# Kernel optimization log

Measured on AMD Instinct MI355X. Metric: run time of the kernel, lower is better.

The kernel has to match this reference:

```python
import jax, jax.numpy as jnp
import numpy as np

D_MODEL = 1024
NUM_HEADS = 16
D_K = D_MODEL // NUM_HEADS
SCALE = float(np.sqrt(D_K))


def setup_inputs() -> dict:
    key = jax.random.key(0)
    ks = jax.random.split(key, 12)
    B, S = 4, 2048
    s = 1.0 / np.sqrt(D_MODEL)
    inp = {
        'query': jax.random.normal(ks[0], (B, S, D_MODEL), jnp.float32),
        'key':   jax.random.normal(ks[1], (B, S, D_MODEL), jnp.float32),
        'value': jax.random.normal(ks[2], (B, S, D_MODEL), jnp.float32),
        'Wq': jax.random.normal(ks[3], (D_MODEL, D_MODEL), jnp.float32) * s,
        'bq': jax.random.normal(ks[4], (D_MODEL,), jnp.float32) * s,
        'Wk': jax.random.normal(ks[5], (D_MODEL, D_MODEL), jnp.float32) * s,
        'bk': jax.random.normal(ks[6], (D_MODEL,), jnp.float32) * s,
        'Wv': jax.random.normal(ks[7], (D_MODEL, D_MODEL), jnp.float32) * s,
        'bv': jax.random.normal(ks[8], (D_MODEL,), jnp.float32) * s,
        'Wo': jax.random.normal(ks[9], (D_MODEL, D_MODEL), jnp.float32) * s,
        'bo': jax.random.normal(ks[10], (D_MODEL,), jnp.float32) * s,
    }
    return inp


def reference(query, key, value, Wq, bq, Wk, bk, Wv, bv, Wo, bo):
    B, Sq, _ = query.shape
    Skv = key.shape[1]
    # torch Linear: x @ W.T + b
    def proj(x, W, b, S):
        y = jnp.einsum('bsd,ed->bse', x, W) + b
        return y.reshape(B, S, NUM_HEADS, D_K).transpose(0, 2, 1, 3)  # [B,H,S,dk]
    Q = proj(query, Wq, bq, Sq)
    K = proj(key, Wk, bk, Skv)
    V = proj(value, Wv, bv, Skv)
    scores = jnp.einsum('bhqd,bhkd->bhqk', Q, K) / SCALE  # [B,H,Sq,Skv]
    attn = jax.nn.softmax(scores, axis=-1)  # dropout=0 -> identity
    out = jnp.einsum('bhqk,bhkd->bhqd', attn, V)
    out = out.transpose(0, 2, 1, 3).reshape(B, Sq, D_MODEL)
    out = jnp.einsum('bsd,ed->bse', out, Wo) + bo
    return out
```

## Files before the change

kernel.cpp:

```cpp
#include <hip/hip_runtime.h>


typedef __attribute__((ext_vector_type(8))) __bf16 bf16x8;
typedef __attribute__((ext_vector_type(4))) __bf16 bf16x4;
typedef __attribute__((ext_vector_type(4))) float f32x4;

#define SCALE_FOLD 0.18033688011112043f

__device__ __forceinline__ void async_copy16(const void* g, void* lds) {
  __builtin_amdgcn_global_load_lds(
      (const __attribute__((address_space(1))) void*)g,
      (__attribute__((address_space(3))) void*)lds, 16, 0, 0);
}

template <int ROWS>
__device__ __forceinline__ void stage_tile(const __bf16* __restrict__ g, int ld,
                                           __bf16* lds, int tid) {
  const int wave_base = tid & ~63;
#pragma unroll
  for (int r = 0; r < ROWS / 32; ++r) {
    int slot = r * 256 + tid;
    int row = slot >> 3;
    int c = slot & 7;
    int gc = c ^ (row & 7);
    async_copy16(g + row * ld + gc * 8, lds + (r * 256 + wave_base) * 8);
  }
}

__device__ __forceinline__ bf16x8 frag_ld(const __bf16* lds, int row, int chunk) {
  return *(const bf16x8*)(lds + row * 64 + ((chunk ^ (row & 7)) << 3));
}

__global__ void cvt3(const float* __restrict__ s0, const float* __restrict__ s1,
                     const float* __restrict__ s2, __bf16* d0, __bf16* d1,
                     __bf16* d2, int n4) {
  const float* src = blockIdx.y == 0 ? s0 : (blockIdx.y == 1 ? s1 : s2);
  __bf16* dst = blockIdx.y == 0 ? d0 : (blockIdx.y == 1 ? d1 : d2);
  int i = blockIdx.x * blockDim.x + threadIdx.x;
  if (i < n4) {
    float4 v = ((const float4*)src)[i];
    bf16x4 o = {(__bf16)v.x, (__bf16)v.y, (__bf16)v.z, (__bf16)v.w};
    ((bf16x4*)dst)[i] = o;
  }
}

__global__ void cvt4(const float* __restrict__ s0, const float* __restrict__ s1,
                     const float* __restrict__ s2, const float* __restrict__ s3,
                     __bf16* d0, __bf16* d1, __bf16* d2, __bf16* d3, int n4) {
  const float* src = blockIdx.y == 0 ? s0
                     : (blockIdx.y == 1 ? s1 : (blockIdx.y == 2 ? s2 : s3));
  __bf16* dst =
      blockIdx.y == 0 ? d0 : (blockIdx.y == 1 ? d1 : (blockIdx.y == 2 ? d2 : d3));
  int i = blockIdx.x * blockDim.x + threadIdx.x;
  if (i < n4) {
    float4 v = ((const float4*)src)[i];
    bf16x4 o = {(__bf16)v.x, (__bf16)v.y, (__bf16)v.z, (__bf16)v.w};
    ((bf16x4*)dst)[i] = o;
  }
}

__device__ __forceinline__ void gemm_body(const __bf16* __restrict__ A,
                                          const __bf16* __restrict__ B,
                                          const float* __restrict__ bias,
                                          void* __restrict__ out, int K,
                                          int mode, int m0, int n0,
                                          __bf16* Alds, __bf16* Blds) {
  const int tid = threadIdx.x;
  const int lane = tid & 63;
  const int w = tid >> 6;
  const int wm = w >> 1, wn = w & 1;
  const int l15 = lane & 15, quad = lane >> 4;

  f32x4 acc[4][4] = {};

  for (int k0 = 0; k0 < K; k0 += 64) {
    stage_tile<128>(A + m0 * K + k0, K, Alds, tid);
    stage_tile<128>(B + n0 * K + k0, K, Blds, tid);
    __syncthreads();
#pragma unroll
    for (int kc = 0; kc < 2; ++kc) {
      bf16x8 af[4], bfr[4];
#pragma unroll
      for (int mi = 0; mi < 4; ++mi)
        af[mi] = frag_ld(Alds, wm * 64 + mi * 16 + l15, kc * 4 + quad);
#pragma unroll
      for (int ni = 0; ni < 4; ++ni)
        bfr[ni] = frag_ld(Blds, wn * 64 + ni * 16 + l15, kc * 4 + quad);
#pragma unroll
      for (int mi = 0; mi < 4; ++mi)
#pragma unroll
        for (int ni = 0; ni < 4; ++ni)
          acc[mi][ni] = __builtin_amdgcn_mfma_f32_16x16x32_bf16(
              af[mi], bfr[ni], acc[mi][ni], 0, 0, 0);
    }
    __syncthreads();
  }

#pragma unroll
  for (int mi = 0; mi < 4; ++mi) {
#pragma unroll
    for (int i = 0; i < 4; ++i) {
      int grow = m0 + wm * 64 + mi * 16 + quad * 4 + i;
#pragma unroll
      for (int ni = 0; ni < 4; ++ni) {
        int gcol = n0 + wn * 64 + ni * 16 + l15;
        float v = acc[mi][ni][i];
        if (mode == 3) {
          v += bias[gcol];
          ((float*)out)[grow * 1024 + gcol] = v;
        } else if (mode == 2) {
          v += bias[grow];
          int h = grow >> 6, dd = grow & 63;
          int b = gcol >> 11, s = gcol & 2047;
          ((__bf16*)out)[(((b * 16 + h) * 64 + dd) * 2048) + s] = (__bf16)v;
        } else {
          v += bias[gcol];
          if (mode == 0) v *= SCALE_FOLD;
          int h = gcol >> 6, dd = gcol & 63;
          int b = grow >> 11, s = grow & 2047;
          ((__bf16*)out)[(((b * 16 + h) * 2048 + s) * 64) + dd] = (__bf16)v;
        }
      }
    }
  }
}

__global__ __launch_bounds__(256) void gemm_qkv(
    const __bf16* __restrict__ xq, const __bf16* __restrict__ xk,
    const __bf16* __restrict__ xv, const __bf16* __restrict__ wq,
    const __bf16* __restrict__ wk, const __bf16* __restrict__ wv,
    const float* __restrict__ bq, const float* __restrict__ bk,
    const float* __restrict__ bv, __bf16* Qb, __bf16* Kb, __bf16* Vtb) {
  __shared__ alignas(16) __bf16 Alds[128 * 64];
  __shared__ alignas(16) __bf16 Blds[128 * 64];
  const int z = blockIdx.z;
  if (z == 0) {
    gemm_body(xq, wq, bq, Qb, 1024, 0, blockIdx.y * 128, blockIdx.x * 128,
              Alds, Blds);
  } else if (z == 1) {
    gemm_body(xk, wk, bk, Kb, 1024, 1, blockIdx.y * 128, blockIdx.x * 128,
              Alds, Blds);
  } else {
    gemm_body(wv, xv, bv, Vtb, 1024, 2, blockIdx.x * 128, blockIdx.y * 128,
              Alds, Blds);
  }
}

__global__ __launch_bounds__(256) void gemm_out(const __bf16* __restrict__ A,
                                                const __bf16* __restrict__ B,
                                                const float* __restrict__ bias,
                                                float* __restrict__ out) {
  __shared__ alignas(16) __bf16 Alds[128 * 64];
  __shared__ alignas(16) __bf16 Blds[128 * 64];
  gemm_body(A, B, bias, out, 1024, 3, blockIdx.y * 128, blockIdx.x * 128, Alds,
            Blds);
}

__global__ __launch_bounds__(256, 2) void attn_kernel(
    const __bf16* __restrict__ Qg, const __bf16* __restrict__ Kg,
    const __bf16* __restrict__ Vt, __bf16* __restrict__ AO) {
  __shared__ alignas(16) __bf16 Klds[2][64 * 64];
  __shared__ alignas(16) __bf16 Vlds[2][64 * 64];
  __shared__ alignas(16) __bf16 PQ[256 * 64];

  const int tid = threadIdx.x;
  const int lane = tid & 63;
  const int w = tid >> 6;
  const int l15 = lane & 15, quad = lane >> 4;
  const int bh = blockIdx.y;
  const int q0 = blockIdx.x * 256;
  const int S = 2048;

  const __bf16* Qbase = Qg + (size_t)bh * S * 64;
  const __bf16* Kbase = Kg + (size_t)bh * S * 64;
  const __bf16* Vbase = Vt + (size_t)bh * 64 * S;

  stage_tile<256>(Qbase + q0 * 64, 64, PQ, tid);
  stage_tile<64>(Kbase, 64, Klds[0], tid);
  stage_tile<64>(Vbase, S, Vlds[0], tid);
  __syncthreads();
  bf16x8 qf[4][2];
#pragma unroll
  for (int qi = 0; qi < 4; ++qi)
#pragma unroll
    for (int kc = 0; kc < 2; ++kc)
      qf[qi][kc] = frag_ld(PQ, w * 64 + qi * 16 + l15, kc * 4 + quad);
  __syncthreads();

  const bf16x8 ones = {__bf16(1.f), __bf16(1.f), __bf16(1.f), __bf16(1.f),
                       __bf16(1.f), __bf16(1.f), __bf16(1.f), __bf16(1.f)};

  f32x4 oacc[4][4] = {};
  f32x4 lacc[4] = {};

  __bf16* Pw = PQ + w * 64 * 64;

  for (int t = 0; t < 32; ++t) {
    const int cur = t & 1;
    if (t + 1 < 32) {
      stage_tile<64>(Kbase + (t + 1) * 64 * 64, 64, Klds[cur ^ 1], tid);
      stage_tile<64>(Vbase + (t + 1) * 64, S, Vlds[cur ^ 1], tid);
    }

    f32x4 sacc[4][4] = {};
#pragma unroll
    for (int kc = 0; kc < 2; ++kc) {
      bf16x8 kf[4];
#pragma unroll
      for (int ci = 0; ci < 4; ++ci)
        kf[ci] = frag_ld(Klds[cur], ci * 16 + l15, kc * 4 + quad);
#pragma unroll
      for (int ci = 0; ci < 4; ++ci)
#pragma unroll
        for (int qi = 0; qi < 4; ++qi)
          sacc[ci][qi] = __builtin_amdgcn_mfma_f32_16x16x32_bf16(
              kf[ci], qf[qi][kc], sacc[ci][qi], 0, 0, 0);
    }

#pragma unroll
    for (int ci = 0; ci < 4; ++ci) {
#pragma unroll
      for (int qi = 0; qi < 4; ++qi) {
        bf16x4 pk;
#pragma unroll
        for (int i = 0; i < 4; ++i)
          pk[i] = (__bf16)__builtin_amdgcn_exp2f(sacc[ci][qi][i]);
        int qrow = qi * 16 + l15;
        int addr = qrow * 64 + (((2 * ci + (quad >> 1)) ^ (qrow & 7)) << 3) +
                   ((quad & 1) << 2);
        *(bf16x4*)(Pw + addr) = pk;
      }
    }

#pragma unroll
    for (int kc = 0; kc < 2; ++kc) {
      bf16x8 pf[4], vf[4];
#pragma unroll
      for (int mi = 0; mi < 4; ++mi)
        pf[mi] = frag_ld(Pw, mi * 16 + l15, kc * 4 + quad);
#pragma unroll
      for (int ni = 0; ni < 4; ++ni)
        vf[ni] = frag_ld(Vlds[cur], ni * 16 + l15, kc * 4 + quad);
#pragma unroll
      for (int mi = 0; mi < 4; ++mi)
        lacc[mi] = __builtin_amdgcn_mfma_f32_16x16x32_bf16(pf[mi], ones,
                                                           lacc[mi], 0, 0, 0);
#pragma unroll
      for (int mi = 0; mi < 4; ++mi)
#pragma unroll
        for (int ni = 0; ni < 4; ++ni)
          oacc[mi][ni] = __builtin_amdgcn_mfma_f32_16x16x32_bf16(
              pf[mi], vf[ni], oacc[mi][ni], 0, 0, 0);
    }
    __syncthreads();
  }

  const int b = bh >> 4;
  const int hh = bh & 15;
#pragma unroll
  for (int mi = 0; mi < 4; ++mi) {
#pragma unroll
    for (int i = 0; i < 4; ++i) {
      int s = q0 + w * 64 + mi * 16 + quad * 4 + i;
      float inv_l = 1.f / lacc[mi][i];
#pragma unroll
      for (int ni = 0; ni < 4; ++ni) {
        int d = ni * 16 + l15;
        AO[((size_t)(b * 2048 + s)) * 1024 + hh * 64 + d] =
            (__bf16)(oacc[mi][ni][i] * inv_l);
      }
    }
  }
}

extern "C" void kernel_launch(void* const* d_in, const int* in_sizes, int n_in,
                              void* d_out, int out_size, void* d_ws,
                              size_t ws_size, hipStream_t stream) {
  const float* q_in = (const float*)d_in[0];
  const float* k_in = (const float*)d_in[1];
  const float* v_in = (const float*)d_in[2];
  const float* Wq = (const float*)d_in[3];
  const float* bq = (const float*)d_in[4];
  const float* Wk = (const float*)d_in[5];
  const float* bk = (const float*)d_in[6];
  const float* Wv = (const float*)d_in[7];
  const float* bv = (const float*)d_in[8];
  const float* Wo = (const float*)d_in[9];
  const float* bo = (const float*)d_in[10];

  const size_t SZ_X = (size_t)8192 * 1024 * 2;
  const size_t SZ_W = (size_t)1024 * 1024 * 2;
  char* p = (char*)d_ws;
  __bf16* xq = (__bf16*)p; p += SZ_X;
  __bf16* xk = (__bf16*)p; p += SZ_X;
  __bf16* xv = (__bf16*)p; p += SZ_X;
  __bf16* wqb = (__bf16*)p; p += SZ_W;
  __bf16* wkb = (__bf16*)p; p += SZ_W;
  __bf16* wvb = (__bf16*)p; p += SZ_W;
  __bf16* wob = (__bf16*)p; p += SZ_W;
  __bf16* Qb = (__bf16*)p; p += SZ_X;
  __bf16* Kb = (__bf16*)p; p += SZ_X;
  __bf16* Vtb = (__bf16*)p; p += SZ_X;
  __bf16* AOb = (__bf16*)p; p += SZ_X;

  const int nx4 = 8192 * 1024 / 4, nw4 = 1024 * 1024 / 4;
  cvt3<<<dim3(nx4 / 256, 3), 256, 0, stream>>>(q_in, k_in, v_in, xq, xk, xv,
                                               nx4);
  cvt4<<<dim3(nw4 / 256, 4), 256, 0, stream>>>(Wq, Wk, Wv, Wo, wqb, wkb, wvb,
                                               wob, nw4);

  gemm_qkv<<<dim3(8, 64, 3), 256, 0, stream>>>(xq, xk, xv, wqb, wkb, wvb, bq,
                                               bk, bv, Qb, Kb, Vtb);

  attn_kernel<<<dim3(8, 64), 256, 0, stream>>>(Qb, Kb, Vtb, AOb);

  gemm_out<<<dim3(8, 64), 256, 0, stream>>>(AOb, wob, bo, (float*)d_out);
}
```

Before: 345.8 us.

## Halve attention query tile per block, split KV tile into sub-steps, merge convert kernels

The attention kernel now handles 128 queries per block (32 per wave) instead of 256. It processes each 64-key tile as two 32-key sub-steps with a much smaller per-wave P buffer in LDS, which cuts LDS use and accumulator registers and doubles the grid to 1024 blocks. This aims for more resident blocks and better CU balance, at the cost of reloading K/V tiles for twice as many blocks and using smaller MFMA batches per step. The two fp32-to-bf16 convert kernels are merged into one launch; the weight slices idle for most of the grid blocks.

After: 360.7 us. 1.04x slower.

```diff
diff --git a/kernel.cpp b/kernel.cpp
--- a/kernel.cpp
+++ b/kernel.cpp
@@ -13,44 +13,46 @@
       (__attribute__((address_space(3))) void*)lds, 16, 0, 0);
 }
 
-template <int ROWS>
+template <int ROWS, int WIDTH>
 __device__ __forceinline__ void stage_tile(const __bf16* __restrict__ g, int ld,
                                            __bf16* lds, int tid) {
+  constexpr int CH = WIDTH / 8;
   const int wave_base = tid & ~63;
 #pragma unroll
-  for (int r = 0; r < ROWS / 32; ++r) {
+  for (int r = 0; r < ROWS * CH / 256; ++r) {
     int slot = r * 256 + tid;
-    int row = slot >> 3;
-    int c = slot & 7;
-    int gc = c ^ (row & 7);
+    int row = slot / CH;
+    int c = slot % CH;
+    int gc = c ^ (row & (CH - 1));
     async_copy16(g + row * ld + gc * 8, lds + (r * 256 + wave_base) * 8);
   }
 }
 
+template <int WIDTH>
 __device__ __forceinline__ bf16x8 frag_ld(const __bf16* lds, int row, int chunk) {
-  return *(const bf16x8*)(lds + row * 64 + ((chunk ^ (row & 7)) << 3));
-}
-
-__global__ void cvt3(const float* __restrict__ s0, const float* __restrict__ s1,
-                     const float* __restrict__ s2, __bf16* d0, __bf16* d1,
-                     __bf16* d2, int n4) {
-  const float* src = blockIdx.y == 0 ? s0 : (blockIdx.y == 1 ? s1 : s2);
-  __bf16* dst = blockIdx.y == 0 ? d0 : (blockIdx.y == 1 ? d1 : d2);
-  int i = blockIdx.x * blockDim.x + threadIdx.x;
-  if (i < n4) {
-    float4 v = ((const float4*)src)[i];
-    bf16x4 o = {(__bf16)v.x, (__bf16)v.y, (__bf16)v.z, (__bf16)v.w};
-    ((bf16x4*)dst)[i] = o;
-  }
-}
-
-__global__ void cvt4(const float* __restrict__ s0, const float* __restrict__ s1,
-                     const float* __restrict__ s2, const float* __restrict__ s3,
-                     __bf16* d0, __bf16* d1, __bf16* d2, __bf16* d3, int n4) {
-  const float* src = blockIdx.y == 0 ? s0
-                     : (blockIdx.y == 1 ? s1 : (blockIdx.y == 2 ? s2 : s3));
-  __bf16* dst =
-      blockIdx.y == 0 ? d0 : (blockIdx.y == 1 ? d1 : (blockIdx.y == 2 ? d2 : d3));
+  return *(const bf16x8*)(lds + row * WIDTH +
+                          ((chunk ^ (row & (WIDTH / 8 - 1))) << 3));
+}
+
+__global__ void cvt_all(const float* __restrict__ s0, const float* __restrict__ s1,
+                        const float* __restrict__ s2, const float* __restrict__ s3,
+                        const float* __restrict__ s4, const float* __restrict__ s5,
+                        const float* __restrict__ s6, __bf16* d0, __bf16* d1,
+                        __bf16* d2, __bf16* d3, __bf16* d4, __bf16* d5,
+                        __bf16* d6, int n4_big, int n4_small) {
+  const int z = blockIdx.y;
+  const float* src;
+  __bf16* dst;
+  int n4;
+  switch (z) {
+    case 0: src = s0; dst = d0; n4 = n4_big; break;
+    case 1: src = s1; dst = d1; n4 = n4_big; break;
+    case 2: src = s2; dst = d2; n4 = n4_big; break;
+    case 3: src = s3; dst = d3; n4 = n4_small; break;
+    case 4: src = s4; dst = d4; n4 = n4_small; break;
+    case 5: src = s5; dst = d5; n4 = n4_small; break;
+    default: src = s6; dst = d6; n4 = n4_small; break;
+  }
   int i = blockIdx.x * blockDim.x + threadIdx.x;
   if (i < n4) {
     float4 v = ((const float4*)src)[i];
@@ -74,18 +76,18 @@
   f32x4 acc[4][4] = {};
 
   for (int k0 = 0; k0 < K; k0 += 64) {
-    stage_tile<128>(A + m0 * K + k0, K, Alds, tid);
-    stage_tile<128>(B + n0 * K + k0, K, Blds, tid);
+    stage_tile<128, 64>(A + m0 * K + k0, K, Alds, tid);
+    stage_tile<128, 64>(B + n0 * K + k0, K, Blds, tid);
     __syncthreads();
 #pragma unroll
     for (int kc = 0; kc < 2; ++kc) {
       bf16x8 af[4], bfr[4];
 #pragma unroll
       for (int mi = 0; mi < 4; ++mi)
-        af[mi] = frag_ld(Alds, wm * 64 + mi * 16 + l15, kc * 4 + quad);
+        af[mi] = frag_ld<64>(Alds, wm * 64 + mi * 16 + l15, kc * 4 + quad);
 #pragma unroll
       for (int ni = 0; ni < 4; ++ni)
-        bfr[ni] = frag_ld(Blds, wn * 64 + ni * 16 + l15, kc * 4 + quad);
+        bfr[ni] = frag_ld<64>(Blds, wn * 64 + ni * 16 + l15, kc * 4 + quad);
 #pragma unroll
       for (int mi = 0; mi < 4; ++mi)
 #pragma unroll
@@ -156,97 +158,101 @@
             Blds);
 }
 
-__global__ __launch_bounds__(256, 2) void attn_kernel(
+__global__ __launch_bounds__(256) void attn_kernel(
     const __bf16* __restrict__ Qg, const __bf16* __restrict__ Kg,
     const __bf16* __restrict__ Vt, __bf16* __restrict__ AO) {
   __shared__ alignas(16) __bf16 Klds[2][64 * 64];
   __shared__ alignas(16) __bf16 Vlds[2][64 * 64];
-  __shared__ alignas(16) __bf16 PQ[256 * 64];
+  __shared__ alignas(16) __bf16 Plds[4][32 * 32];
 
   const int tid = threadIdx.x;
   const int lane = tid & 63;
   const int w = tid >> 6;
   const int l15 = lane & 15, quad = lane >> 4;
   const int bh = blockIdx.y;
-  const int q0 = blockIdx.x * 256;
+  const int q0 = blockIdx.x * 128;
   const int S = 2048;
 
   const __bf16* Qbase = Qg + (size_t)bh * S * 64;
   const __bf16* Kbase = Kg + (size_t)bh * S * 64;
   const __bf16* Vbase = Vt + (size_t)bh * 64 * S;
 
-  stage_tile<256>(Qbase + q0 * 64, 64, PQ, tid);
-  stage_tile<64>(Kbase, 64, Klds[0], tid);
-  stage_tile<64>(Vbase, S, Vlds[0], tid);
+  stage_tile<128, 64>(Qbase + q0 * 64, 64, (__bf16*)Klds, tid);
   __syncthreads();
-  bf16x8 qf[4][2];
-#pragma unroll
-  for (int qi = 0; qi < 4; ++qi)
+  bf16x8 qf[2][2];
+#pragma unroll
+  for (int qi = 0; qi < 2; ++qi)
 #pragma unroll
     for (int kc = 0; kc < 2; ++kc)
-      qf[qi][kc] = frag_ld(PQ, w * 64 + qi * 16 + l15, kc * 4 + quad);
+      qf[qi][kc] =
+          frag_ld<64>((__bf16*)Klds, w * 32 + qi * 16 + l15, kc * 4 + quad);
+  __syncthreads();
+
+  stage_tile<64, 64>(Kbase, 64, Klds[0], tid);
+  stage_tile<64, 64>(Vbase, S, Vlds[0], tid);
   __syncthreads();
 
   const bf16x8 ones = {__bf16(1.f), __bf16(1.f), __bf16(1.f), __bf16(1.f),
                        __bf16(1.f), __bf16(1.f), __bf16(1.f), __bf16(1.f)};
 
-  f32x4 oacc[4][4] = {};
-  f32x4 lacc[4] = {};
-
-  __bf16* Pw = PQ + w * 64 * 64;
-
-  for (int t = 0; t < 32; ++t) {
-    const int cur = t & 1;
-    if (t + 1 < 32) {
-      stage_tile<64>(Kbase + (t + 1) * 64 * 64, 64, Klds[cur ^ 1], tid);
-      stage_tile<64>(Vbase + (t + 1) * 64, S, Vlds[cur ^ 1], tid);
-    }
-
-    f32x4 sacc[4][4] = {};
-#pragma unroll
-    for (int kc = 0; kc < 2; ++kc) {
-      bf16x8 kf[4];
-#pragma unroll
-      for (int ci = 0; ci < 4; ++ci)
-        kf[ci] = frag_ld(Klds[cur], ci * 16 + l15, kc * 4 + quad);
-#pragma unroll
-      for (int ci = 0; ci < 4; ++ci)
-#pragma unroll
-        for (int qi = 0; qi < 4; ++qi)
-          sacc[ci][qi] = __builtin_amdgcn_mfma_f32_16x16x32_bf16(
-              kf[ci], qf[qi][kc], sacc[ci][qi], 0, 0, 0);
-    }
-
-#pragma unroll
-    for (int ci = 0; ci < 4; ++ci) {
-#pragma unroll
-      for (int qi = 0; qi < 4; ++qi) {
-        bf16x4 pk;
-#pragma unroll
-        for (int i = 0; i < 4; ++i)
-          pk[i] = (__bf16)__builtin_amdgcn_exp2f(sacc[ci][qi][i]);
-        int qrow = qi * 16 + l15;
-        int addr = qrow * 64 + (((2 * ci + (quad >> 1)) ^ (qrow & 7)) << 3) +
-                   ((quad & 1) << 2);
-        *(bf16x4*)(Pw + addr) = pk;
+  f32x4 oacc[2][4] = {};
+  f32x4 lacc[2] = {};
+  __bf16* Pw = Plds[w];
+
+  for (int mt = 0; mt < 32; ++mt) {
+    const int cur = mt & 1;
+    if (mt + 1 < 32) {
+      stage_tile<64, 64>(Kbase + (mt + 1) * 64 * 64, 64, Klds[cur ^ 1], tid);
+      stage_tile<64, 64>(Vbase + (mt + 1) * 64, S, Vlds[cur ^ 1], tid);
+    }
+
+#pragma unroll
+    for (int sub = 0; sub < 2; ++sub) {
+      f32x4 sacc[2][2] = {};
+#pragma unroll
+      for (int kc = 0; kc < 2; ++kc) {
+        bf16x8 kf[2];
+#pragma unroll
+        for (int ci = 0; ci < 2; ++ci)
+          kf[ci] =
+              frag_ld<64>(Klds[cur], sub * 32 + ci * 16 + l15, kc * 4 + quad);
+#pragma unroll
+        for (int ci = 0; ci < 2; ++ci)
+#pragma unroll
+          for (int qi = 0; qi < 2; ++qi)
+            sacc[ci][qi] = __builtin_amdgcn_mfma_f32_16x16x32_bf16(
+                kf[ci], qf[qi][kc], sacc[ci][qi], 0, 0, 0);
       }
-    }
-
-#pragma unroll
-    for (int kc = 0; kc < 2; ++kc) {
-      bf16x8 pf[4], vf[4];
-#pragma unroll
-      for (int mi = 0; mi < 4; ++mi)
-        pf[mi] = frag_ld(Pw, mi * 16 + l15, kc * 4 + quad);
+
+#pragma unroll
+      for (int ci = 0; ci < 2; ++ci) {
+#pragma unroll
+        for (int qi = 0; qi < 2; ++qi) {
+          bf16x4 pk;
+#pragma unroll
+          for (int i = 0; i < 4; ++i)
+            pk[i] = (__bf16)__builtin_amdgcn_exp2f(sacc[ci][qi][i]);
+          int qrow = qi * 16 + l15;
+          int addr = qrow * 32 +
+                     ((((ci << 1) + (quad >> 1)) ^ (qrow & 3)) << 3) +
+                     ((quad & 1) << 2);
+          *(bf16x4*)(Pw + addr) = pk;
+        }
+      }
+
+      bf16x8 pf[2], vf[4];
+#pragma unroll
+      for (int mi = 0; mi < 2; ++mi)
+        pf[mi] = frag_ld<32>(Pw, mi * 16 + l15, quad);
 #pragma unroll
       for (int ni = 0; ni < 4; ++ni)
-        vf[ni] = frag_ld(Vlds[cur], ni * 16 + l15, kc * 4 + quad);
-#pragma unroll
-      for (int mi = 0; mi < 4; ++mi)
+        vf[ni] = frag_ld<64>(Vlds[cur], ni * 16 + l15, sub * 4 + quad);
+#pragma unroll
+      for (int mi = 0; mi < 2; ++mi)
         lacc[mi] = __builtin_amdgcn_mfma_f32_16x16x32_bf16(pf[mi], ones,
                                                            lacc[mi], 0, 0, 0);
 #pragma unroll
-      for (int mi = 0; mi < 4; ++mi)
+      for (int mi = 0; mi < 2; ++mi)
 #pragma unroll
         for (int ni = 0; ni < 4; ++ni)
           oacc[mi][ni] = __builtin_amdgcn_mfma_f32_16x16x32_bf16(
@@ -258,10 +264,10 @@
   const int b = bh >> 4;
   const int hh = bh & 15;
 #pragma unroll
-  for (int mi = 0; mi < 4; ++mi) {
+  for (int mi = 0; mi < 2; ++mi) {
 #pragma unroll
     for (int i = 0; i < 4; ++i) {
-      int s = q0 + w * 64 + mi * 16 + quad * 4 + i;
+      int s = q0 + w * 32 + mi * 16 + quad * 4 + i;
       float inv_l = 1.f / lacc[mi][i];
 #pragma unroll
       for (int ni = 0; ni < 4; ++ni) {
@@ -304,15 +310,14 @@
   __bf16* AOb = (__bf16*)p; p += SZ_X;
 
   const int nx4 = 8192 * 1024 / 4, nw4 = 1024 * 1024 / 4;
-  cvt3<<<dim3(nx4 / 256, 3), 256, 0, stream>>>(q_in, k_in, v_in, xq, xk, xv,
-                                               nx4);
-  cvt4<<<dim3(nw4 / 256, 4), 256, 0, stream>>>(Wq, Wk, Wv, Wo, wqb, wkb, wvb,
-                                               wob, nw4);
+  cvt_all<<<dim3(nx4 / 256, 7), 256, 0, stream>>>(
+      q_in, k_in, v_in, Wq, Wk, Wv, Wo, xq, xk, xv, wqb, wkb, wvb, wob, nx4,
+      nw4);
 
   gemm_qkv<<<dim3(8, 64, 3), 256, 0, stream>>>(xq, xk, xv, wqb, wkb, wvb, bq,
                                                bk, bv, Qb, Kb, Vtb);
 
-  attn_kernel<<<dim3(8, 64), 256, 0, stream>>>(Qb, Kb, Vtb, AOb);
+  attn_kernel<<<dim3(16, 64), 256, 0, stream>>>(Qb, Kb, Vtb, AOb);
 
   gemm_out<<<dim3(8, 64), 256, 0, stream>>>(AOb, wob, bo, (float*)d_out);
 }
```
